# Kernel optimization log

Measured on AMD Instinct MI355X. Metric: run time of the kernel, lower is better.

Reference implementation:

```python
import jax, jax.numpy as jnp
import numpy as np

SHAPES = ((100, 152), (50, 76), (25, 38), (13, 19))  # (H, W) per feature level, strides 8/16/32/64 of 800x1216
S_TOTAL = sum(h * w for h, w in SHAPES)  # 20197
B, D, NH, NL, NP, NLAYERS, DFF = 2, 256, 8, 4, 4, 6, 1024
HD = D // NH


def _layernorm(x, g, b):
    m = x.mean(-1, keepdims=True)
    v = ((x - m) ** 2).mean(-1, keepdims=True)
    return (x - m) * jax.lax.rsqrt(v + 1e-5) * g + b


def _get_reference_points(valid_ratios):
    # valid_ratios: (B, NL, 2) as (w_ratio, h_ratio)
    refs = []
    for lvl, (Hl, Wl) in enumerate(SHAPES):
        ry, rx = jnp.meshgrid(jnp.linspace(0.5, Hl - 0.5, Hl), jnp.linspace(0.5, Wl - 0.5, Wl), indexing='ij')
        ry = ry.reshape(-1)[None] / (valid_ratios[:, None, lvl, 1] * Hl)
        rx = rx.reshape(-1)[None] / (valid_ratios[:, None, lvl, 0] * Wl)
        refs.append(jnp.stack([rx, ry], -1))
    ref = jnp.concatenate(refs, 1)                    # (B, S, 2)
    return ref[:, :, None] * valid_ratios[:, None]    # (B, S, NL, 2)


def _sample_level(v, loc, Hl, Wl):
    # v: (B, Hl*Wl, NH, HD); loc: (B, Lq, NH, NP, 2) normalized coords in [0,1]
    # matches F.grid_sample(align_corners=False, padding_mode='zeros'): px = loc_x*W - 0.5
    px = loc[..., 0] * Wl - 0.5
    py = loc[..., 1] * Hl - 0.5
    x0 = jnp.floor(px)
    y0 = jnp.floor(py)
    lx = px - x0
    ly = py - y0
    x0i = x0.astype(jnp.int32)
    y0i = y0.astype(jnp.int32)
    b_idx = jnp.arange(v.shape[0])[:, None, None, None]
    h_idx = jnp.arange(NH)[None, None, :, None]
    out = jnp.zeros(px.shape + (HD,), v.dtype)
    for dx, dy, w in ((0, 0, (1 - lx) * (1 - ly)), (1, 0, lx * (1 - ly)), (0, 1, (1 - lx) * ly), (1, 1, lx * ly)):
        xi = x0i + dx
        yi = y0i + dy
        valid = (xi >= 0) & (xi < Wl) & (yi >= 0) & (yi < Hl)
        idx = jnp.clip(yi, 0, Hl - 1) * Wl + jnp.clip(xi, 0, Wl - 1)
        g = v[b_idx, idx, h_idx]                      # (B, Lq, NH, NP, HD)
        out = out + g * (w * valid)[..., None]
    return out


def _msda(q, ref, src, Wv, bv, Woff, boff, Wa, ba, Wo, bo):
    # Multi-scale deformable attention (2D reference points).
    Bq, Lq, _ = q.shape
    value = (src @ Wv + bv).reshape(Bq, S_TOTAL, NH, HD)
    off = (q @ Woff + boff).reshape(Bq, Lq, NH, NL, NP, 2)
    attn = jax.nn.softmax((q @ Wa + ba).reshape(Bq, Lq, NH, NL * NP), -1).reshape(Bq, Lq, NH, NL, NP)
    normalizer = jnp.array([[w, h] for h, w in SHAPES], jnp.float32)  # (NL, 2) as (W, H)
    locs = ref[:, :, None, :, None, :] + off / normalizer[None, None, None, :, None, :]
    acc = jnp.zeros((Bq, Lq, NH, HD), q.dtype)
    start = 0
    for l, (Hl, Wl) in enumerate(SHAPES):
        v = value[:, start:start + Hl * Wl]
        start += Hl * Wl
        s = _sample_level(v, locs[:, :, :, l], Hl, Wl)
        acc = acc + jnp.einsum('blhp,blhpd->blhd', attn[:, :, :, l], s)
    return acc.reshape(Bq, Lq, D) @ Wo + bo


def setup_inputs() -> dict:
    key = jax.random.key(0)
    ks = jax.random.split(key, 12)
    sc = 0.02
    def w(k, shape):
        return jax.random.normal(k, shape, jnp.float32) * sc
    return {
        'src': jax.random.normal(ks[0], (B, S_TOTAL, D), jnp.float32),
        'pos': jax.random.normal(ks[1], (B, S_TOTAL, D), jnp.float32) * 0.1,
        'valid_ratios': jnp.ones((B, NL, 2), jnp.float32),
        'W_value': w(ks[2], (NLAYERS, D, D)), 'b_value': jnp.zeros((NLAYERS, D), jnp.float32),
        'W_off': w(ks[3], (NLAYERS, D, NH * NL * NP * 2)), 'b_off': w(ks[4], (NLAYERS, NH * NL * NP * 2)),
        'W_attn': w(ks[5], (NLAYERS, D, NH * NL * NP)), 'b_attn': jnp.zeros((NLAYERS, NH * NL * NP), jnp.float32),
        'W_out': w(ks[6], (NLAYERS, D, D)), 'b_out': jnp.zeros((NLAYERS, D), jnp.float32),
        'ln1_g': jnp.ones((NLAYERS, D), jnp.float32), 'ln1_b': jnp.zeros((NLAYERS, D), jnp.float32),
        'W_ff1': w(ks[7], (NLAYERS, D, DFF)), 'b_ff1': jnp.zeros((NLAYERS, DFF), jnp.float32),
        'W_ff2': w(ks[8], (NLAYERS, DFF, D)), 'b_ff2': jnp.zeros((NLAYERS, D), jnp.float32),
        'ln2_g': jnp.ones((NLAYERS, D), jnp.float32), 'ln2_b': jnp.zeros((NLAYERS, D), jnp.float32),
    }


def reference(src, pos, valid_ratios, W_value, b_value, W_off, b_off, W_attn, b_attn, W_out, b_out, ln1_g, ln1_b, W_ff1, b_ff1, W_ff2, b_ff2, ln2_g, ln2_b):
    ref = _get_reference_points(valid_ratios)
    out = src
    for i in range(NLAYERS):
        q = out + pos
        a = _msda(q, ref, out, W_value[i], b_value[i], W_off[i], b_off[i], W_attn[i], b_attn[i], W_out[i], b_out[i])
        out = _layernorm(out + a, ln1_g[i], ln1_b[i])
        f = jax.nn.relu(out @ W_ff1[i] + b_ff1[i]) @ W_ff2[i] + b_ff2[i]
        out = _layernorm(out + f, ln2_g[i], ln2_b[i])
    return out
```

## Files before the change

kernel.cpp:

```cpp
#include <hip/hip_runtime.h>
#include <math.h>

#define B_N   2
#define S_N   20197
#define M_N   (B_N * S_N)
#define D_N   256
#define NH_N  8
#define HD_N  32
#define DFF_N 1024

typedef __attribute__((ext_vector_type(8))) short short8;
typedef __attribute__((ext_vector_type(4))) float f32x4;

__device__ __forceinline__ unsigned short f2bf(float f)
{
    unsigned u = __builtin_bit_cast(unsigned, f);
    u += 0x7fffu + ((u >> 16) & 1u);
    return (unsigned short)(u >> 16);
}
__device__ __forceinline__ float bf2f(unsigned short s)
{
    return __builtin_bit_cast(float, ((unsigned)s) << 16);
}

__global__ void compute_ref_kernel(const float* __restrict__ vr, float* __restrict__ refpts)
{
    int q = blockIdx.x * blockDim.x + threadIdx.x;
    if (q >= M_N) return;
    int b = q / S_N;
    int s = q - b * S_N;
    const int Hs[4] = {100, 50, 25, 13};
    const int Ws[4] = {152, 76, 38, 19};
    int l0, i, j;
    if (s < 15200)      { l0 = 0; i = s / 152; j = s - i * 152; }
    else if (s < 19000) { int t = s - 15200; l0 = 1; i = t / 76; j = t - i * 76; }
    else if (s < 19950) { int t = s - 19000; l0 = 2; i = t / 38; j = t - i * 38; }
    else                { int t = s - 19950; l0 = 3; i = t / 19; j = t - i * 19; }
    float ry = (i + 0.5f) / (vr[(b * 4 + l0) * 2 + 1] * (float)Hs[l0]);
    float rx = (j + 0.5f) / (vr[(b * 4 + l0) * 2 + 0] * (float)Ws[l0]);
#pragma unroll
    for (int l = 0; l < 4; ++l) {
        refpts[(size_t)q * 8 + l * 2 + 0] = rx * vr[(b * 4 + l) * 2 + 0];
        refpts[(size_t)q * 8 + l * 2 + 1] = ry * vr[(b * 4 + l) * 2 + 1];
    }
}

__global__ __launch_bounds__(256) void transpose_w_kernel(
    const float* __restrict__ W, unsigned short* __restrict__ Wt,
    int K, int Nsrc, int dstN, int rowOff)
{
    __shared__ float t[32][33];
    const float* Wl = W + (size_t)blockIdx.z * K * Nsrc;
    unsigned short* Wtl = Wt + (size_t)blockIdx.z * K * dstN;
    int n0 = blockIdx.x * 32, k0 = blockIdx.y * 32;
    int tx = threadIdx.x & 31, ty = threadIdx.x >> 5;
#pragma unroll
    for (int r = 0; r < 32; r += 8)
        t[ty + r][tx] = Wl[(size_t)(k0 + ty + r) * Nsrc + n0 + tx];
    __syncthreads();
#pragma unroll
    for (int r = 0; r < 32; r += 8)
        Wtl[(size_t)(rowOff + n0 + ty + r) * K + k0 + tx] = f2bf(t[tx][ty + r]);
}

__global__ void boa_kernel(const float* __restrict__ boff, const float* __restrict__ ba,
                           float* __restrict__ boa)
{
    int i = blockIdx.x, j = threadIdx.x;
    boa[i * 384 + j] = (j < 256) ? boff[i * 256 + j] : ba[i * 128 + j - 256];
}

__global__ __launch_bounds__(256) void init_kernel(
    const float* __restrict__ src, const float* __restrict__ pos,
    float* __restrict__ out, unsigned short* __restrict__ outb,
    unsigned short* __restrict__ qb)
{
    size_t i = (size_t)blockIdx.x * 256 + threadIdx.x;
    float s = src[i];
    out[i]  = s;
    outb[i] = f2bf(s);
    qb[i]   = f2bf(s + pos[i]);
}

__global__ __launch_bounds__(256) void gemm_bf16(
    const unsigned short* __restrict__ A, const unsigned short* __restrict__ Wt,
    const float* __restrict__ bias, unsigned short* __restrict__ C,
    int M, int N, int K, int mode)
{
    __shared__ short As[128 * 72];
    __shared__ short Bs[128 * 72];
    const int tid  = threadIdx.x;
    const int m0   = blockIdx.x * 128, n0 = blockIdx.y * 128;
    const int lane = tid & 63, wave = tid >> 6;
    const int wm   = (wave & 1) * 64, wn = (wave >> 1) * 64;
    const int quad = lane >> 4, lm = lane & 15;
    f32x4 acc[4][4] = {};
    const int ar = tid >> 1, ac = (tid & 1) * 32;
    const int gm = m0 + ar;

    for (int k0 = 0; k0 < K; k0 += 64) {
        short8 s[4];
        if (gm < M) {
            const unsigned short* ap = A + (size_t)gm * K + k0 + ac;
#pragma unroll
            for (int i = 0; i < 4; ++i) s[i] = *(const short8*)(ap + 8 * i);
        } else {
#pragma unroll
            for (int i = 0; i < 4; ++i) s[i] = short8{0,0,0,0,0,0,0,0};
        }
        short* da = &As[ar * 72 + ac];
#pragma unroll
        for (int i = 0; i < 4; ++i) *(short8*)(da + i * 8) = s[i];
        const unsigned short* wp = Wt + (size_t)(n0 + ar) * K + k0 + ac;
        short* db = &Bs[ar * 72 + ac];
#pragma unroll
        for (int i = 0; i < 4; ++i) *(short8*)(db + i * 8) = *(const short8*)(wp + i * 8);
        __syncthreads();
#pragma unroll
        for (int ks = 0; ks < 2; ++ks) {
            short8 af[4], bf[4];
#pragma unroll
            for (int mi = 0; mi < 4; ++mi)
                af[mi] = *(short8*)&As[(wm + mi * 16 + lm) * 72 + ks * 32 + quad * 8];
#pragma unroll
            for (int ni = 0; ni < 4; ++ni)
                bf[ni] = *(short8*)&Bs[(wn + ni * 16 + lm) * 72 + ks * 32 + quad * 8];
#pragma unroll
            for (int mi = 0; mi < 4; ++mi)
#pragma unroll
                for (int ni = 0; ni < 4; ++ni)
                    acc[mi][ni] = __builtin_amdgcn_mfma_f32_16x16x32_bf16(
                        af[mi], bf[ni], acc[mi][ni], 0, 0, 0);
        }
        __syncthreads();
    }
    const bool dorelu = (mode == 2);
#pragma unroll
    for (int ni = 0; ni < 4; ++ni) {
        int gc = n0 + wn + ni * 16 + lm;
        float bb = bias[gc];
#pragma unroll
        for (int mi = 0; mi < 4; ++mi)
#pragma unroll
            for (int j = 0; j < 4; ++j) {
                int gr = m0 + wm + mi * 16 + quad * 4 + j;
                if (gr < M) {
                    float v = acc[mi][ni][j] + bb;
                    if (dorelu) v = fmaxf(v, 0.f);
                    C[(size_t)gr * N + gc] = f2bf(v);
                }
            }
    }
}

__global__ __launch_bounds__(256, 2) void gemm_bf16_ln(
    const unsigned short* __restrict__ A, const unsigned short* __restrict__ Wt,
    const float* __restrict__ bias, float* __restrict__ out,
    unsigned short* __restrict__ outb, const float* __restrict__ g,
    const float* __restrict__ beta, const float* __restrict__ pos,
    unsigned short* __restrict__ qb, int M, int K)
{
    __shared__ short As[128 * 72];
    __shared__ short Bs[256 * 72];
    __shared__ float red[128][4];
    __shared__ float mstat[128][2];
    const int tid  = threadIdx.x;
    const int m0   = blockIdx.x * 128;
    const int lane = tid & 63, wave = tid >> 6;
    const int wm   = (wave & 1) * 64, wn = (wave >> 1) * 128;
    const int quad = lane >> 4, lm = lane & 15;
    f32x4 acc[4][8] = {};
    const int ar = tid >> 1, ac = (tid & 1) * 32;
    const int gm = m0 + ar;

    for (int k0 = 0; k0 < K; k0 += 64) {
        short8 s[4];
        if (gm < M) {
            const unsigned short* ap = A + (size_t)gm * K + k0 + ac;
#pragma unroll
            for (int i = 0; i < 4; ++i) s[i] = *(const short8*)(ap + 8 * i);
        } else {
#pragma unroll
            for (int i = 0; i < 4; ++i) s[i] = short8{0,0,0,0,0,0,0,0};
        }
        short* da = &As[ar * 72 + ac];
#pragma unroll
        for (int i = 0; i < 4; ++i) *(short8*)(da + i * 8) = s[i];
        const unsigned short* wp = Wt + (size_t)tid * K + k0;
        short* db = &Bs[tid * 72];
#pragma unroll
        for (int i = 0; i < 8; ++i) *(short8*)(db + i * 8) = *(const short8*)(wp + i * 8);
        __syncthreads();
#pragma unroll
        for (int ks = 0; ks < 2; ++ks) {
            short8 af[4], bf[8];
#pragma unroll
            for (int mi = 0; mi < 4; ++mi)
                af[mi] = *(short8*)&As[(wm + mi * 16 + lm) * 72 + ks * 32 + quad * 8];
#pragma unroll
            for (int ni = 0; ni < 8; ++ni)
                bf[ni] = *(short8*)&Bs[(wn + ni * 16 + lm) * 72 + ks * 32 + quad * 8];
#pragma unroll
            for (int mi = 0; mi < 4; ++mi)
#pragma unroll
                for (int ni = 0; ni < 8; ++ni)
                    acc[mi][ni] = __builtin_amdgcn_mfma_f32_16x16x32_bf16(
                        af[mi], bf[ni], acc[mi][ni], 0, 0, 0);
        }
        __syncthreads();
    }
    float g8[8], b8[8], bi8[8];
#pragma unroll
    for (int ni = 0; ni < 8; ++ni) {
        int gc = wn + ni * 16 + lm;
        g8[ni] = g[gc]; b8[ni] = beta[gc]; bi8[ni] = bias[gc];
    }
#pragma unroll
    for (int mi = 0; mi < 4; ++mi)
#pragma unroll
        for (int j = 0; j < 4; ++j) {
            int r  = wm + mi * 16 + quad * 4 + j;
            int gr = m0 + r;
            float s = 0.f, sq = 0.f;
            if (gr < M) {
#pragma unroll
                for (int ni = 0; ni < 8; ++ni) {
                    float v = acc[mi][ni][j] + bi8[ni] + out[(size_t)gr * 256 + wn + ni * 16 + lm];
                    acc[mi][ni][j] = v;
                    s += v; sq += v * v;
                }
            }
#pragma unroll
            for (int o = 1; o < 16; o <<= 1) {
                s  += __shfl_xor(s, o, 64);
                sq += __shfl_xor(sq, o, 64);
            }
            if (lm == 0) { red[r][(wn >> 7) * 2 + 0] = s; red[r][(wn >> 7) * 2 + 1] = sq; }
        }
    __syncthreads();
    if (tid < 128) {
        float S = red[tid][0] + red[tid][2];
        float Q = red[tid][1] + red[tid][3];
        float mean = S * (1.f / 256.f);
        float var  = Q * (1.f / 256.f) - mean * mean;
        mstat[tid][0] = mean;
        mstat[tid][1] = rsqrtf(var + 1e-5f);
    }
    __syncthreads();
#pragma unroll
    for (int mi = 0; mi < 4; ++mi)
#pragma unroll
        for (int j = 0; j < 4; ++j) {
            int r  = wm + mi * 16 + quad * 4 + j;
            int gr = m0 + r;
            if (gr >= M) continue;
            float mean = mstat[r][0], rs = mstat[r][1];
#pragma unroll
            for (int ni = 0; ni < 8; ++ni) {
                size_t idx = (size_t)gr * 256 + wn + ni * 16 + lm;
                float v = (acc[mi][ni][j] - mean) * rs * g8[ni] + b8[ni];
                out[idx]  = v;
                outb[idx] = f2bf(v);
                if (qb) qb[idx] = f2bf(v + pos[idx]);
            }
        }
}

__global__ __launch_bounds__(256) void msda_sample_kernel(
    const unsigned short* __restrict__ value,
    const unsigned short* __restrict__ oa,
    const float* __restrict__ refpts,
    unsigned short* __restrict__ accb)
{
    __shared__ int pts[272 * 10];
    const int tid = threadIdx.x;
    const int q0  = blockIdx.x * 2;
    {
        const int qq = tid >> 7;
        const int q  = q0 + qq;
        const int jj = tid & 127;
        const int h  = jj >> 4, l = (jj >> 2) & 3, t = jj & 15;
        const int b  = q / S_N;
        const int Wi = 152 >> l;
        const int Hi = (100 >> l) + (l == 3);
        const float Wf = (float)Wi, Hf = (float)Hi;
        const int start = (l < 1) ? 0 : (l < 2) ? 15200 : (l < 3) ? 19000 : 19950;
        const unsigned short* oq = oa + (size_t)q * 384;
        unsigned op = *(const unsigned*)(oq + jj * 2);
        float ox = __builtin_bit_cast(float, op << 16);
        float oy = __builtin_bit_cast(float, op & 0xffff0000u);
        float2 rp = *(const float2*)(refpts + (size_t)q * 8 + l * 2);
        float logit = bf2f(oq[256 + jj]);
        float mx = logit;
#pragma unroll
        for (int o = 1; o < 16; o <<= 1) mx = fmaxf(mx, __shfl_xor(mx, o, 64));
        float e = expf(logit - mx);
        float sum = e;
#pragma unroll
        for (int o = 1; o < 16; o <<= 1) sum += __shfl_xor(sum, o, 64);
        float w = e / sum;
        float px = (rp.x + ox / Wf) * Wf - 0.5f;
        float py = (rp.y + oy / Hf) * Hf - 0.5f;
        float x0f = floorf(px), y0f = floorf(py);
        float fx = px - x0f, fy = py - y0f;
        int x0 = (int)x0f, y0 = (int)y0f;
        int base = b * S_N + start;
        int P = qq * 136 + h * 17 + t;
#pragma unroll
        for (int c = 0; c < 4; ++c) {
            int dx = c & 1, dy = c >> 1;
            int xi = x0 + dx, yi = y0 + dy;
            bool valid = (xi >= 0) & (xi < Wi) & (yi >= 0) & (yi < Hi);
            int xc = min(max(xi, 0), Wi - 1);
            int yc = min(max(yi, 0), Hi - 1);
            float cw = (dx ? fx : 1.f - fx) * (dy ? fy : 1.f - fy);
            int offby = ((base + yc * Wi + xc) * 256 + h * 32) * 2;
            pts[P * 10 + c * 2 + 0] = offby;
            pts[P * 10 + c * 2 + 1] = __builtin_bit_cast(int, valid ? w * cw : 0.f);
        }
    }
    __syncthreads();
    const int qq = tid >> 7;
    const int gl = tid & 127;
    const int hh = gl >> 4, lg = gl & 15;
    const int cn = lg & 3;
    const int c8 = (lg >> 2) * 8;
    const char* vb = (const char*)value + c8 * 2;
    float a[8] = {};
    const int Pb = qq * 136 + hh * 17;
#pragma unroll
    for (int t = 0; t < 16; ++t) {
        int2 ow = *(const int2*)&pts[(Pb + t) * 10 + cn * 2];
        float w = __builtin_bit_cast(float, ow.y);
        short8 v8 = *(const short8*)(vb + ow.x);
#pragma unroll
        for (int i = 0; i < 8; ++i)
            a[i] = fmaf(w, bf2f((unsigned short)v8[i]), a[i]);
    }
#pragma unroll
    for (int o = 1; o < 4; o <<= 1)
#pragma unroll
        for (int i = 0; i < 8; ++i) a[i] += __shfl_xor(a[i], o, 64);
    if (cn == 0) {
        int4 pk;
        pk.x = (int)((unsigned)f2bf(a[0]) | ((unsigned)f2bf(a[1]) << 16));
        pk.y = (int)((unsigned)f2bf(a[2]) | ((unsigned)f2bf(a[3]) << 16));
        pk.z = (int)((unsigned)f2bf(a[4]) | ((unsigned)f2bf(a[5]) << 16));
        pk.w = (int)((unsigned)f2bf(a[6]) | ((unsigned)f2bf(a[7]) << 16));
        *(int4*)((char*)accb + ((size_t)(q0 + qq) * 256 + hh * 32 + c8) * 2) = pk;
    }
}

extern "C" void kernel_launch(void* const* d_in, const int* in_sizes, int n_in,
                              void* d_out, int out_size, void* d_ws, size_t ws_size,
                              hipStream_t stream)
{
    const float* src  = (const float*)d_in[0];
    const float* pos  = (const float*)d_in[1];
    const float* vr   = (const float*)d_in[2];
    const float* Wv   = (const float*)d_in[3];
    const float* bv   = (const float*)d_in[4];
    const float* Woff = (const float*)d_in[5];
    const float* boff = (const float*)d_in[6];
    const float* Wa   = (const float*)d_in[7];
    const float* ba   = (const float*)d_in[8];
    const float* Wo   = (const float*)d_in[9];
    const float* bo   = (const float*)d_in[10];
    const float* g1   = (const float*)d_in[11];
    const float* be1  = (const float*)d_in[12];
    const float* W1   = (const float*)d_in[13];
    const float* b1   = (const float*)d_in[14];
    const float* W2   = (const float*)d_in[15];
    const float* b2   = (const float*)d_in[16];
    const float* g2   = (const float*)d_in[17];
    const float* be2  = (const float*)d_in[18];

    float* out = (float*)d_out;
    float* ws  = (float*)d_ws;
    float* refpts = ws;
    float* valreg = refpts + 323200;
    float* oareg  = valreg + 5170432;
    float* slack  = oareg  + 7755648;
    float* accreg = slack  + 7755648;
    float* qreg   = accreg + 5170432;
    float* obreg  = qreg   + 5170432;
    unsigned short* value_bf = (unsigned short*)valreg;
    unsigned short* oa       = (unsigned short*)oareg;
    unsigned short* hidden   = (unsigned short*)valreg;
    unsigned short* accb     = (unsigned short*)accreg;
    unsigned short* qb       = (unsigned short*)qreg;
    unsigned short* outb     = (unsigned short*)obreg;
    unsigned short* wtv  = (unsigned short*)(obreg + 5170432);
    unsigned short* wtoa = wtv  + 6 * 65536;
    unsigned short* wto  = wtoa + 6 * 98304;
    unsigned short* wt1  = wto  + 6 * 65536;
    unsigned short* wt2  = wt1  + 6 * 262144;
    float* boa = (float*)(wt2 + 6 * 262144);

    dim3 blk(256);
    compute_ref_kernel<<<(M_N + 255) / 256, 256, 0, stream>>>(vr, refpts);
    init_kernel<<<M_N, blk, 0, stream>>>(src, pos, out, outb, qb);
    transpose_w_kernel<<<dim3(8, 8, 6),  blk, 0, stream>>>(Wv,   wtv,  256, 256,  256, 0);
    transpose_w_kernel<<<dim3(8, 8, 6),  blk, 0, stream>>>(Woff, wtoa, 256, 256,  384, 0);
    transpose_w_kernel<<<dim3(4, 8, 6),  blk, 0, stream>>>(Wa,   wtoa, 256, 128,  384, 256);
    transpose_w_kernel<<<dim3(8, 8, 6),  blk, 0, stream>>>(Wo,   wto,  256, 256,  256, 0);
    transpose_w_kernel<<<dim3(32, 8, 6), blk, 0, stream>>>(W1,   wt1,  256, 1024, 1024, 0);
    transpose_w_kernel<<<dim3(8, 32, 6), blk, 0, stream>>>(W2,   wt2,  1024, 256, 256, 0);
    boa_kernel<<<6, 384, 0, stream>>>(boff, ba, boa);

    const int mt = (M_N + 127) / 128;
    for (int i = 0; i < 6; ++i) {
        gemm_bf16<<<dim3(mt, 3), blk, 0, stream>>>(qb, wtoa + (size_t)i * 98304,
                                                   boa + i * 384, oa, M_N, 384, 256, 1);
        gemm_bf16<<<dim3(mt, 2), blk, 0, stream>>>(outb, wtv + (size_t)i * 65536,
                                                   bv + i * 256, value_bf, M_N, 256, 256, 1);
        msda_sample_kernel<<<M_N / 2, blk, 0, stream>>>(value_bf, oa, refpts, accb);
        gemm_bf16_ln<<<mt, blk, 0, stream>>>(accb, wto + (size_t)i * 65536, bo + i * 256,
                                             out, outb, g1 + i * 256, be1 + i * 256,
                                             nullptr, nullptr, M_N, 256);
        gemm_bf16<<<dim3(mt, 8), blk, 0, stream>>>(outb, wt1 + (size_t)i * 262144,
                                                   b1 + i * 1024, hidden, M_N, 1024, 256, 2);
        gemm_bf16_ln<<<mt, blk, 0, stream>>>(hidden, wt2 + (size_t)i * 262144, b2 + i * 256,
                                             out, outb, g2 + i * 256, be2 + i * 256,
                                             pos, qb, M_N, 1024);
    }
}
```

Baseline: 2.601 ms.

## Restructure deformable sampling: one query per block, swizzled order, batched gathers

The sampling kernel now handles one query per 128-thread block instead of two per 256-thread block. Block indices are remapped so consecutive blocks stride across eight chunks of queries, which on MI355X spreads neighbouring queries across XCDs, presumably to improve L2 locality for the gathered value rows. The inner loop issues eight independent 16-byte gathers before accumulating, and uses packed float2 multiply-adds, to raise memory-level parallelism. Smaller blocks double the block count, and the remap could hurt locality if the XCD assignment assumption is wrong.

```diff
diff --git a/kernel.cpp b/kernel.cpp
--- a/kernel.cpp
+++ b/kernel.cpp
@@ -11,6 +11,7 @@
 
 typedef __attribute__((ext_vector_type(8))) short short8;
 typedef __attribute__((ext_vector_type(4))) float f32x4;
+typedef __attribute__((ext_vector_type(2))) float f32x2;
 
 __device__ __forceinline__ unsigned short f2bf(float f)
 {
@@ -266,19 +267,19 @@
         }
 }
 
-__global__ __launch_bounds__(256) void msda_sample_kernel(
+#define CHUNK_B ((M_N + 7) / 8)
+__global__ __launch_bounds__(128) void msda_sample_kernel(
     const unsigned short* __restrict__ value,
     const unsigned short* __restrict__ oa,
     const float* __restrict__ refpts,
     unsigned short* __restrict__ accb)
 {
-    __shared__ int pts[272 * 10];
+    __shared__ int pts[136 * 10];
+    const int q = (blockIdx.x & 7) * CHUNK_B + (blockIdx.x >> 3);
+    if (q >= M_N) return;
     const int tid = threadIdx.x;
-    const int q0  = blockIdx.x * 2;
     {
-        const int qq = tid >> 7;
-        const int q  = q0 + qq;
-        const int jj = tid & 127;
+        const int jj = tid;
         const int h  = jj >> 4, l = (jj >> 2) & 3, t = jj & 15;
         const int b  = q / S_N;
         const int Wi = 152 >> l;
@@ -305,7 +306,7 @@
         float fx = px - x0f, fy = py - y0f;
         int x0 = (int)x0f, y0 = (int)y0f;
         int base = b * S_N + start;
-        int P = qq * 136 + h * 17 + t;
+        int P = h * 17 + t;
 #pragma unroll
         for (int c = 0; c < 4; ++c) {
             int dx = c & 1, dy = c >> 1;
@@ -320,34 +321,55 @@
         }
     }
     __syncthreads();
-    const int qq = tid >> 7;
-    const int gl = tid & 127;
-    const int hh = gl >> 4, lg = gl & 15;
+    const int hh = tid >> 4, lg = tid & 15;
     const int cn = lg & 3;
     const int c8 = (lg >> 2) * 8;
     const char* vb = (const char*)value + c8 * 2;
-    float a[8] = {};
-    const int Pb = qq * 136 + hh * 17;
-#pragma unroll
-    for (int t = 0; t < 16; ++t) {
-        int2 ow = *(const int2*)&pts[(Pb + t) * 10 + cn * 2];
-        float w = __builtin_bit_cast(float, ow.y);
-        short8 v8 = *(const short8*)(vb + ow.x);
+    f32x2 a[4] = {};
+    const int Pb = hh * 17;
+#pragma unroll
+    for (int t0 = 0; t0 < 16; t0 += 8) {
+        int2 ow[8];
 #pragma unroll
         for (int i = 0; i < 8; ++i)
-            a[i] = fmaf(w, bf2f((unsigned short)v8[i]), a[i]);
+            ow[i] = *(const int2*)&pts[(Pb + t0 + i) * 10 + cn * 2];
+        int4 v[8];
+#pragma unroll
+        for (int i = 0; i < 8; ++i)
+            v[i] = *(const int4*)(vb + ow[i].x);
+#pragma unroll
+        for (int i = 0; i < 8; ++i) {
+            float w = __builtin_bit_cast(float, ow[i].y);
+            f32x2 wv = {w, w};
+            unsigned d;
+            d = (unsigned)v[i].x;
+            a[0] += wv * f32x2{__builtin_bit_cast(float, d << 16),
+                               __builtin_bit_cast(float, d & 0xffff0000u)};
+            d = (unsigned)v[i].y;
+            a[1] += wv * f32x2{__builtin_bit_cast(float, d << 16),
+                               __builtin_bit_cast(float, d & 0xffff0000u)};
+            d = (unsigned)v[i].z;
+            a[2] += wv * f32x2{__builtin_bit_cast(float, d << 16),
+                               __builtin_bit_cast(float, d & 0xffff0000u)};
+            d = (unsigned)v[i].w;
+            a[3] += wv * f32x2{__builtin_bit_cast(float, d << 16),
+                               __builtin_bit_cast(float, d & 0xffff0000u)};
+        }
     }
 #pragma unroll
     for (int o = 1; o < 4; o <<= 1)
 #pragma unroll
-        for (int i = 0; i < 8; ++i) a[i] += __shfl_xor(a[i], o, 64);
+        for (int i = 0; i < 4; ++i) {
+            a[i].x += __shfl_xor(a[i].x, o, 64);
+            a[i].y += __shfl_xor(a[i].y, o, 64);
+        }
     if (cn == 0) {
         int4 pk;
-        pk.x = (int)((unsigned)f2bf(a[0]) | ((unsigned)f2bf(a[1]) << 16));
-        pk.y = (int)((unsigned)f2bf(a[2]) | ((unsigned)f2bf(a[3]) << 16));
-        pk.z = (int)((unsigned)f2bf(a[4]) | ((unsigned)f2bf(a[5]) << 16));
-        pk.w = (int)((unsigned)f2bf(a[6]) | ((unsigned)f2bf(a[7]) << 16));
-        *(int4*)((char*)accb + ((size_t)(q0 + qq) * 256 + hh * 32 + c8) * 2) = pk;
+        pk.x = (int)((unsigned)f2bf(a[0].x) | ((unsigned)f2bf(a[0].y) << 16));
+        pk.y = (int)((unsigned)f2bf(a[1].x) | ((unsigned)f2bf(a[1].y) << 16));
+        pk.z = (int)((unsigned)f2bf(a[2].x) | ((unsigned)f2bf(a[2].y) << 16));
+        pk.w = (int)((unsigned)f2bf(a[3].x) | ((unsigned)f2bf(a[3].y) << 16));
+        *(int4*)((char*)accb + ((size_t)q * 256 + hh * 32 + c8) * 2) = pk;
     }
 }
 
@@ -414,7 +436,7 @@
                                                    boa + i * 384, oa, M_N, 384, 256, 1);
         gemm_bf16<<<dim3(mt, 2), blk, 0, stream>>>(outb, wtv + (size_t)i * 65536,
                                                    bv + i * 256, value_bf, M_N, 256, 256, 1);
-        msda_sample_kernel<<<M_N / 2, blk, 0, stream>>>(value_bf, oa, refpts, accb);
+        msda_sample_kernel<<<8 * CHUNK_B, dim3(128), 0, stream>>>(value_bf, oa, refpts, accb);
         gemm_bf16_ln<<<mt, blk, 0, stream>>>(accb, wto + (size_t)i * 65536, bo + i * 256,
                                              out, outb, g1 + i * 256, be1 + i * 256,
                                              nullptr, nullptr, M_N, 256);
```

After: 2.615 ms. Within noise of the previous version (+0.5%).
